# Kernel tuning notes

Hardware: AMD Instinct MI355X
Metric: run time of the kernel (lower is better)

Reference implementation:

```python
import jax, jax.numpy as jnp
import numpy as np

B, LQ, LK, DQ, DK, DV = 8, 2048, 2048, 1024, 1024, 1024
TOP_K = 64
NEG_INF = float('-inf')


def setup_inputs() -> dict:
    key = jax.random.key(0)
    kq, kk, kv, km, kw = jax.random.split(key, 5)
    queries = jax.random.normal(kq, (B, LQ, DQ), dtype=jnp.float32)
    keys = jax.random.normal(kk, (B, LK, DK), dtype=jnp.float32)
    values = jax.random.normal(kv, (B, LK, DV), dtype=jnp.float32)
    mask = jax.random.randint(km, (B, LQ, LK), 0, 2, dtype=jnp.int32)
    # nn.Linear(query_dim, key_dim, bias=False) weight: [key_dim, query_dim]
    W = jax.random.normal(kw, (DK, DQ), dtype=jnp.float32) / np.sqrt(DQ)
    return {"queries": queries, "keys": keys, "values": values,
            "mask": mask, "W": W, "top_k": TOP_K}


def reference(queries, keys, values, mask, W, top_k):
    # scores = (queries @ W.T) @ keys^T  -> [B, LQ, LK]  (method='general')
    q_proj = jnp.einsum('bqd,kd->bqk', queries, W)  # [B, LQ, DK]
    scores = jnp.einsum('bqd,btd->bqt', q_proj, keys)  # [B, LQ, LK]
    scores = jnp.where(mask == 0, NEG_INF, scores)
    alphas = jax.nn.softmax(scores, axis=-1)
    alphas = jnp.where(jnp.isnan(alphas), 0.0, alphas)  # fully-masked rows -> 0
    # top-k: zero out non-top-k probabilities, then re-softmax over the
    # resulting tensor (zeros contribute exp(0)=1, matching torch semantics)
    _, idx = jax.lax.top_k(alphas, top_k)  # [B, LQ, top_k]
    b_idx = jnp.arange(alphas.shape[0])[:, None, None]
    q_idx = jnp.arange(alphas.shape[1])[None, :, None]
    topk_mask = jnp.zeros(alphas.shape, alphas.dtype).at[b_idx, q_idx, idx].set(1.0)
    alphas = jnp.where(topk_mask == 0, 0.0, alphas)
    alphas = jax.nn.softmax(alphas, axis=-1)
    alphas = jnp.where(jnp.isnan(alphas), 0.0, alphas)
    # dropout_rate = 0.0 -> identity
    return jnp.einsum('bqt,btd->bqd', alphas, values)  # [B, LQ, DV]
```

## Files before the change

### kernel.cpp

```cpp
#include <hip/hip_runtime.h>
#include <math.h>

#define BATCH 8
#define SEQ   2048
#define DIM   1024
#define TOPK  64
#define NEGMASK -1e30f
#define CAND_THRESH 16.0f
#define CAP 28

typedef _Float16 f16;
typedef _Float16 f16x8 __attribute__((ext_vector_type(8)));
typedef float f32x4 __attribute__((ext_vector_type(4)));

__device__ __forceinline__ void async_load16(const void* g, void* l) {
  __builtin_amdgcn_global_load_lds(
      (const __attribute__((address_space(1))) void*)g,
      (__attribute__((address_space(3))) void*)l, 16, 0, 0);
}

__global__ __launch_bounds__(256) void pack_mask_kernel(
    const int4* __restrict__ mask4, unsigned long long* __restrict__ mb) {
  const int wave = threadIdx.x >> 6, lane = threadIdx.x & 63;
  const size_t nGrp = (size_t)16384 * 8;
  for (size_t g = (size_t)blockIdx.x * 8 + wave * 2; g < nGrp; g += 2048 * 8) {
    int4 v0 = mask4[g * 64 + lane];
    int4 v1 = mask4[(g + 1) * 64 + lane];
    unsigned long long a0 = __ballot(v0.x != 0);
    unsigned long long a1 = __ballot(v0.y != 0);
    unsigned long long a2 = __ballot(v0.z != 0);
    unsigned long long a3 = __ballot(v0.w != 0);
    unsigned long long b0 = __ballot(v1.x != 0);
    unsigned long long b1 = __ballot(v1.y != 0);
    unsigned long long b2 = __ballot(v1.z != 0);
    unsigned long long b3 = __ballot(v1.w != 0);
    if (lane == 0) {
      mb[g * 4 + 0] = a0; mb[g * 4 + 1] = a1;
      mb[g * 4 + 2] = a2; mb[g * 4 + 3] = a3;
      mb[g * 4 + 4] = b0; mb[g * 4 + 5] = b1;
      mb[g * 4 + 6] = b2; mb[g * 4 + 7] = b3;
    }
  }
}

__global__ __launch_bounds__(256) void colsum_partial_kernel(
    const float* __restrict__ values, float* __restrict__ partial) {
  int bid = blockIdx.x;
  int tc = bid >> 5;
  int b  = (bid >> 2) & 7;
  int dg = bid & 3;
  int d  = dg * 256 + threadIdx.x;
  const float* vp = values + ((size_t)b * SEQ + (size_t)tc * 256) * DIM + d;
  float s = 0.f;
  #pragma unroll 8
  for (int t = 0; t < 256; ++t) s += vp[(size_t)t * DIM];
  partial[((size_t)tc * BATCH + b) * DIM + d] = s;
}

__global__ __launch_bounds__(256) void colsum_reduce_kernel(
    const float* __restrict__ partial, float* __restrict__ colsum) {
  int idx = blockIdx.x * 256 + threadIdx.x;
  float s = 0.f;
  #pragma unroll
  for (int tc = 0; tc < 8; ++tc) s += partial[(size_t)tc * 8192 + idx];
  colsum[idx] = s;
}

__global__ __launch_bounds__(256) void cvt_f32_to_f16(
    const float* __restrict__ in, f16* __restrict__ out, int n) {
  int i = (blockIdx.x * 256 + threadIdx.x) * 4;
  if (i >= n) return;
  float4 v = *(const float4*)(in + i);
  union { f16 h[4]; uint2 u; } pk;
  pk.h[0] = (f16)v.x; pk.h[1] = (f16)v.y; pk.h[2] = (f16)v.z; pk.h[3] = (f16)v.w;
  *(uint2*)(out + i) = pk.u;
}


#define GEMM_PROLOGUE(APTR, BPTR)                                           \
  const int tid = threadIdx.x;                                              \
  const int wave = tid >> 6, lane = tid & 63;                               \
  const int wm = (wave >> 1) * 64, wn = (wave & 1) * 64;                    \
  const int r0 = wave * 32 + (lane >> 2);                                   \
  const int c16 = (lane & 3) ^ ((r0 >> 1) & 3);                            \
  const f16* srcA0 = (APTR) + (size_t)(m0 + r0) * DIM + c16 * 8;           \
  const f16* srcA1 = (APTR) + (size_t)(m0 + r0 + 16) * DIM + c16 * 8;      \
  const f16* srcB0 = (BPTR) + (size_t)(n0 + r0) * DIM + c16 * 8;           \
  const f16* srcB1 = (BPTR) + (size_t)(n0 + r0 + 16) * DIM + c16 * 8;      \
  int offA[4], offB[4];                                                     \
  _Pragma("unroll")                                                         \
  for (int i = 0; i < 4; ++i) {                                             \
    int r = wm + i * 16 + (lane & 15);                                      \
    offA[i] = r * 64 + ((lane >> 4) ^ ((r >> 1) & 3)) * 16;                 \
    int rn = wn + i * 16 + (lane & 15);                                     \
    offB[i] = rn * 64 + ((lane >> 4) ^ ((rn >> 1) & 3)) * 16;               \
  }                                                                         \
  f32x4 acc[4][4];                                                          \
  _Pragma("unroll")                                                         \
  for (int i = 0; i < 4; ++i)                                               \
    _Pragma("unroll")                                                       \
    for (int j = 0; j < 4; ++j)                                             \
      acc[i][j] = (f32x4){0.f, 0.f, 0.f, 0.f};                              \
                                    \
  async_load16(srcA0, smA + wave * 2048);                                   \
  async_load16(srcA1, smA + wave * 2048 + 1024);                            \
  async_load16(srcB0, smB + wave * 2048);                                   \
  async_load16(srcB1, smB + wave * 2048 + 1024);                            \
  __syncthreads();                                                          \
  int cur = 0;                                                              \
  for (int k0 = 0; k0 < DIM; k0 += 32) {                                    \
    const int nxt = cur ^ 1;                                                \
    if (k0 + 32 < DIM) {                                                    \
      async_load16(srcA0 + k0 + 32, smA + nxt * 8192 + wave * 2048);        \
      async_load16(srcA1 + k0 + 32, smA + nxt * 8192 + wave * 2048 + 1024); \
      async_load16(srcB0 + k0 + 32, smB + nxt * 8192 + wave * 2048);        \
      async_load16(srcB1 + k0 + 32, smB + nxt * 8192 + wave * 2048 + 1024); \
    }                                                                       \
    f16x8 af[4], bf[4];                                                     \
    _Pragma("unroll")                                                       \
    for (int i = 0; i < 4; ++i) {                                           \
      af[i] = *(const f16x8*)(smA + cur * 8192 + offA[i]);                  \
      bf[i] = *(const f16x8*)(smB + cur * 8192 + offB[i]);                  \
    }                                                                       \
    _Pragma("unroll")                                                       \
    for (int i = 0; i < 4; ++i)                                             \
      _Pragma("unroll")                                                     \
      for (int j = 0; j < 4; ++j)                                           \
        acc[i][j] = __builtin_amdgcn_mfma_f32_16x16x32_f16(                 \
            af[i], bf[j], acc[i][j], 0, 0, 0);                              \
    __syncthreads();   \
    cur = nxt;                                                              \
  }

__global__ __launch_bounds__(256, 3) void gemm_qproj(
    const f16* __restrict__ A, const f16* __restrict__ Bw,
    f16* __restrict__ C) {
  __shared__ __align__(128) char smA[16384];
  __shared__ __align__(128) char smB[16384];
  const int swz = (blockIdx.x & 7) * 128 + (blockIdx.x >> 3);
  const int m0 = (swz >> 3) * 128;
  const int n0 = (swz & 7) * 128;
  GEMM_PROLOGUE(A, Bw)
  const int cr = m0 + wm + (lane >> 4) * 4;
  const int cc = n0 + wn + (lane & 15);
  #pragma unroll
  for (int i = 0; i < 4; ++i)
    #pragma unroll
    for (int j = 0; j < 4; ++j)
      #pragma unroll
      for (int reg = 0; reg < 4; ++reg)
        C[(size_t)(cr + i * 16 + reg) * DIM + cc + j * 16] = (f16)acc[i][j][reg];
}

__global__ __launch_bounds__(256, 3) void gemm_scores(
    const f16* __restrict__ QP, const f16* __restrict__ K16,
    const unsigned long long* __restrict__ maskbits,
    float2* __restrict__ cand,
    int* __restrict__ counts) {
  __shared__ __align__(128) char smA[16384];
  __shared__ __align__(128) char smB[16384];
  const int swz = (blockIdx.x & 7) * 256 + (blockIdx.x >> 3);
  const int m0 = (swz >> 4) * 128;
  const int n0 = (swz & 15) * 128;
  const int b  = m0 >> 11;
  const f16* Bk = K16 + (size_t)b * SEQ * DIM;
  GEMM_PROLOGUE(QP, Bk)

  const int g  = lane >> 4;
  const int lc = lane & 15;

  const int grp = (n0 + wn) >> 8;
  const int basebit = ((n0 + wn) & 255) >> 2;
  #pragma unroll
  for (int i = 0; i < 4; ++i)
    #pragma unroll
    for (int reg = 0; reg < 4; ++reg) {
      const int r = wm + i * 16 + g * 4 + reg;
      const unsigned long long mw =
          maskbits[(size_t)(m0 + r) * 32 + grp * 4 + (lc & 3)];
      #pragma unroll
      for (int j = 0; j < 4; ++j)
        if (!((mw >> (basebit + j * 4 + (lc >> 2))) & 1ull))
          acc[i][j][reg] = NEGMASK;
    }

  float* hm = (float*)smA;
  #pragma unroll
  for (int i = 0; i < 4; ++i)
    #pragma unroll
    for (int reg = 0; reg < 4; ++reg) {
      const int r = wm + i * 16 + g * 4 + reg;
      float m4 = fmaxf(fmaxf(acc[i][0][reg], acc[i][1][reg]),
                       fmaxf(acc[i][2][reg], acc[i][3][reg]));
      #pragma unroll
      for (int off = 8; off >= 1; off >>= 1) m4 = fmaxf(m4, __shfl_xor(m4, off));
      if (lc == 0) hm[r * 2 + (wn >> 6)] = m4;
    }
  __syncthreads();

  const int pairbase = (n0 >> 7) * 2 + (wn >> 6);
  #pragma unroll
  for (int i = 0; i < 4; ++i)
    #pragma unroll
    for (int reg = 0; reg < 4; ++reg) {
      const int r = wm + i * 16 + g * 4 + reg;
      const float tm = fmaxf(hm[r * 2], hm[r * 2 + 1]);
      const float thresh = fmaxf(tm - CAND_THRESH, -1e29f);
      float2* slot = cand + ((size_t)(m0 + r) * 32 + pairbase) * CAP;
      int cnt = 0;
      #pragma unroll
      for (int j = 0; j < 4; ++j) {
        const float s = acc[i][j][reg];
        const bool c = s > thresh;
        const unsigned long long bal = __ballot(c);
        const int seg = (int)((bal >> (g * 16)) & 0xFFFFull);
        const int pos = cnt + __popc(seg & ((1 << lc) - 1));
        if (c && pos < CAP) {
          float2 e; e.x = s; e.y = __int_as_float(n0 + wn + j * 16 + lc);
          slot[pos] = e;
        }
        cnt += __popc(seg);
      }
      if (lc == 0) counts[(size_t)(m0 + r) * 32 + pairbase] = cnt < CAP ? cnt : CAP;
    }
}

__global__ __launch_bounds__(512) void topk_kernel(
    const float2* __restrict__ cand,
    const int*    __restrict__ counts,
    const float*  __restrict__ values,
    const float*  __restrict__ colsum,
    float* __restrict__ out)
{
  __shared__ float ssc[8][128];
  __shared__ int   sidx[8][128];
  const int wave = threadIdx.x >> 6;
  const int lane = threadIdx.x & 63;
  const int grow = blockIdx.x * 8 + wave;
  const int b    = grow >> 11;
  float* msc = ssc[wave];
  int*   mix = sidx[wave];

  int cnt_p = 0;
  if (lane < 32) cnt_p = counts[(size_t)grow * 32 + lane];
  const float2* myslots = cand + ((size_t)grow * 32 + lane) * CAP;

  float mv = -3e38f;
  for (int k = 0; k < cnt_p; ++k) mv = fmaxf(mv, myslots[k].x);
  #pragma unroll
  for (int off = 32; off > 0; off >>= 1) mv = fmaxf(mv, __shfl_xor(mv, off));
  const bool dead = (mv <= -1e29f);

  float total_g = 0.f;
  f32x4 oacc[4];
  #pragma unroll
  for (int j = 0; j < 4; ++j) oacc[j] = (f32x4){0.f, 0.f, 0.f, 0.f};
  const float* vbase = values + (size_t)b * SEQ * DIM;

  if (!dead) {
    const float thresh = mv - CAND_THRESH;
    int f = 0; float zp = 0.f;
    for (int k = 0; k < cnt_p; ++k) {
      float s = myslots[k].x;
      if (s > thresh) { ++f; zp += __expf(s - mv); }
    }
    int incl = f;
    #pragma unroll
    for (int off = 1; off < 64; off <<= 1) {
      int t = __shfl_up(incl, off);
      if (lane >= off) incl += t;
    }
    const int base = incl - f;
    const int F = __shfl(incl, 63);
    #pragma unroll
    for (int off = 32; off > 0; off >>= 1) zp += __shfl_xor(zp, off);
    const float Z = zp;
    int w = 0;
    for (int k = 0; k < cnt_p; ++k) {
      float2 cv = myslots[k];
      if (cv.x > thresh) {
        int p = base + w;
        if (p < 128) { msc[p] = cv.x; mix[p] = __float_as_int(cv.y); }
        ++w;
      }
    }
    asm volatile("s_waitcnt lgkmcnt(0)" ::: "memory");

    if (F <= TOPK) {
      for (int c = 0; c < F; ++c) {
        float g = expm1f(__expf(msc[c] - mv) / Z);
        total_g += g;
        const float* vrow = vbase + (size_t)mix[c] * DIM;
        #pragma unroll
        for (int j = 0; j < 4; ++j) {
          f32x4 v = *(const f32x4*)(vrow + j * 256 + lane * 4);
          #pragma unroll
          for (int e = 0; e < 4; ++e) oacc[j][e] = fmaf(g, v[e], oacc[j][e]);
        }
      }
    } else {
      const int nlist = F < 128 ? F : 128;
      for (int itk = 0; itk < TOPK; ++itk) {
        float bv = -3e38f; int bi = 1 << 30; int bsl = -1;
        #pragma unroll
        for (int h = 0; h < 2; ++h) {
          int sl = lane + h * 64;
          if (sl < nlist) {
            float v = msc[sl]; int id = mix[sl];
            if (v > bv || (v == bv && id < bi)) { bv = v; bi = id; bsl = sl; }
          }
        }
        #pragma unroll
        for (int off = 32; off > 0; off >>= 1) {
          float ov = __shfl_xor(bv, off);
          int   oi = __shfl_xor(bi, off);
          int   os = __shfl_xor(bsl, off);
          if (ov > bv || (ov == bv && oi < bi)) { bv = ov; bi = oi; bsl = os; }
        }
        if (bv <= -1e29f) break;
        float g = expm1f(__expf(bv - mv) / Z);
        total_g += g;
        const float* vrow = vbase + (size_t)bi * DIM;
        #pragma unroll
        for (int j = 0; j < 4; ++j) {
          f32x4 v = *(const f32x4*)(vrow + j * 256 + lane * 4);
          #pragma unroll
          for (int e = 0; e < 4; ++e) oacc[j][e] = fmaf(g, v[e], oacc[j][e]);
        }
        if (lane == 0) msc[bsl] = -3e38f;
        asm volatile("s_waitcnt lgkmcnt(0)" ::: "memory");
      }
    }
  }

  const float inv = 1.0f / (2048.0f + total_g);
  const float* cs = colsum + (size_t)b * DIM;
  float* orow = out + (size_t)grow * DIM;
  #pragma unroll
  for (int j = 0; j < 4; ++j) {
    f32x4 c = *(const f32x4*)(cs + j * 256 + lane * 4);
    f32x4 o;
    #pragma unroll
    for (int e = 0; e < 4; ++e) o[e] = (c[e] + oacc[j][e]) * inv;
    *(f32x4*)(orow + j * 256 + lane * 4) = o;
  }
}

extern "C" void kernel_launch(void* const* d_in, const int* in_sizes, int n_in,
                              void* d_out, int out_size, void* d_ws, size_t ws_size,
                              hipStream_t stream) {
  const float* queries = (const float*)d_in[0];
  const float* keys    = (const float*)d_in[1];
  const float* values  = (const float*)d_in[2];
  const int*   mask    = (const int*)d_in[3];
  const float* W       = (const float*)d_in[4];
  float* out = (float*)d_out;

  char* base = (char*)d_ws;
  float2* cand   = (float2*)base;
  f16*   q16     = (f16*)base;
  f16*   w16     = (f16*)(base + (size_t)32 * 1024 * 1024);
  int*   counts  = (int*)(base + (size_t)112 * 1024 * 1024);
  unsigned long long* maskbits =
      (unsigned long long*)(base + (size_t)114 * 1024 * 1024);
  f16*   qp16    = (f16*)(base + (size_t)128 * 1024 * 1024);
  f16*   k16     = (f16*)(base + (size_t)160 * 1024 * 1024);
  float* colsum  = (float*)(base + (size_t)192 * 1024 * 1024);
  float* partial = colsum + 8192;

  pack_mask_kernel<<<2048, 256, 0, stream>>>((const int4*)mask, maskbits);
  colsum_partial_kernel<<<256, 256, 0, stream>>>(values, partial);
  colsum_reduce_kernel<<<32, 256, 0, stream>>>(partial, colsum);
  cvt_f32_to_f16<<<16384, 256, 0, stream>>>(queries, q16, 16384 * 1024);
  cvt_f32_to_f16<<<1024, 256, 0, stream>>>(W, w16, 1024 * 1024);
  gemm_qproj<<<1024, 256, 0, stream>>>(q16, w16, qp16);
  cvt_f32_to_f16<<<16384, 256, 0, stream>>>(keys, k16, 16384 * 1024);
  gemm_scores<<<2048, 256, 0, stream>>>(qp16, k16, maskbits, cand, counts);
  topk_kernel<<<2048, 512, 0, stream>>>(cand, counts, values, colsum, out);
}
```

Before: 317.8 us.

## Shrink GEMM tiles to 128x64 and merge prep kernels into two launches

Both GEMMs now use 128x64 output tiles with 24 KB of shared memory and a launch bound of 4 blocks. Each wave owns a 32x64 strip, so the cross-wave max exchange and extra barrier in the scores epilogue go away, and the candidate threshold becomes the max of each 64-column chunk. The mask packing, column sums and f32-to-f16 conversions are folded into two multi-role kernels to cut launch count and let independent prep work overlap. In exchange each A tile is reloaded from global memory twice as often, and the per-chunk threshold may admit more candidates before the CAP limit.

```diff
diff --git a/kernel.cpp b/kernel.cpp
--- a/kernel.cpp
+++ b/kernel.cpp
@@ -19,209 +19,203 @@
       (__attribute__((address_space(3))) void*)l, 16, 0, 0);
 }
 
-__global__ __launch_bounds__(256) void pack_mask_kernel(
-    const int4* __restrict__ mask4, unsigned long long* __restrict__ mb) {
-  const int wave = threadIdx.x >> 6, lane = threadIdx.x & 63;
-  const size_t nGrp = (size_t)16384 * 8;
-  for (size_t g = (size_t)blockIdx.x * 8 + wave * 2; g < nGrp; g += 2048 * 8) {
-    int4 v0 = mask4[g * 64 + lane];
-    int4 v1 = mask4[(g + 1) * 64 + lane];
-    unsigned long long a0 = __ballot(v0.x != 0);
-    unsigned long long a1 = __ballot(v0.y != 0);
-    unsigned long long a2 = __ballot(v0.z != 0);
-    unsigned long long a3 = __ballot(v0.w != 0);
-    unsigned long long b0 = __ballot(v1.x != 0);
-    unsigned long long b1 = __ballot(v1.y != 0);
-    unsigned long long b2 = __ballot(v1.z != 0);
-    unsigned long long b3 = __ballot(v1.w != 0);
-    if (lane == 0) {
-      mb[g * 4 + 0] = a0; mb[g * 4 + 1] = a1;
-      mb[g * 4 + 2] = a2; mb[g * 4 + 3] = a3;
-      mb[g * 4 + 4] = b0; mb[g * 4 + 5] = b1;
-      mb[g * 4 + 6] = b2; mb[g * 4 + 7] = b3;
-    }
-  }
-}
-
-__global__ __launch_bounds__(256) void colsum_partial_kernel(
-    const float* __restrict__ values, float* __restrict__ partial) {
-  int bid = blockIdx.x;
-  int tc = bid >> 5;
-  int b  = (bid >> 2) & 7;
-  int dg = bid & 3;
-  int d  = dg * 256 + threadIdx.x;
-  const float* vp = values + ((size_t)b * SEQ + (size_t)tc * 256) * DIM + d;
-  float s = 0.f;
-  #pragma unroll 8
-  for (int t = 0; t < 256; ++t) s += vp[(size_t)t * DIM];
-  partial[((size_t)tc * BATCH + b) * DIM + d] = s;
-}
-
-__global__ __launch_bounds__(256) void colsum_reduce_kernel(
-    const float* __restrict__ partial, float* __restrict__ colsum) {
-  int idx = blockIdx.x * 256 + threadIdx.x;
-  float s = 0.f;
-  #pragma unroll
-  for (int tc = 0; tc < 8; ++tc) s += partial[(size_t)tc * 8192 + idx];
-  colsum[idx] = s;
-}
-
-__global__ __launch_bounds__(256) void cvt_f32_to_f16(
-    const float* __restrict__ in, f16* __restrict__ out, int n) {
-  int i = (blockIdx.x * 256 + threadIdx.x) * 4;
-  if (i >= n) return;
-  float4 v = *(const float4*)(in + i);
-  union { f16 h[4]; uint2 u; } pk;
-  pk.h[0] = (f16)v.x; pk.h[1] = (f16)v.y; pk.h[2] = (f16)v.z; pk.h[3] = (f16)v.w;
-  *(uint2*)(out + i) = pk.u;
-}
-
+__global__ __launch_bounds__(256) void prep1_kernel(
+    const float* __restrict__ queries, const float* __restrict__ W,
+    const int4* __restrict__ mask4, const float* __restrict__ values,
+    f16* __restrict__ q16, f16* __restrict__ w16,
+    unsigned long long* __restrict__ mb, float* __restrict__ partial) {
+  const int blk = blockIdx.x;
+  if (blk < 16384) {
+    int i = (blk * 256 + threadIdx.x) * 4;
+    float4 v = *(const float4*)(queries + i);
+    union { f16 h[4]; uint2 u; } pk;
+    pk.h[0] = (f16)v.x; pk.h[1] = (f16)v.y; pk.h[2] = (f16)v.z; pk.h[3] = (f16)v.w;
+    *(uint2*)(q16 + i) = pk.u;
+  } else if (blk < 17408) {
+    int i = ((blk - 16384) * 256 + threadIdx.x) * 4;
+    float4 v = *(const float4*)(W + i);
+    union { f16 h[4]; uint2 u; } pk;
+    pk.h[0] = (f16)v.x; pk.h[1] = (f16)v.y; pk.h[2] = (f16)v.z; pk.h[3] = (f16)v.w;
+    *(uint2*)(w16 + i) = pk.u;
+  } else if (blk < 19456) {
+    const int bid = blk - 17408;
+    const int wave = threadIdx.x >> 6, lane = threadIdx.x & 63;
+    const size_t nGrp = (size_t)16384 * 8;
+    for (size_t g = (size_t)bid * 8 + wave * 2; g < nGrp; g += 2048 * 8) {
+      int4 v0 = mask4[g * 64 + lane];
+      int4 v1 = mask4[(g + 1) * 64 + lane];
+      unsigned long long a0 = __ballot(v0.x != 0);
+      unsigned long long a1 = __ballot(v0.y != 0);
+      unsigned long long a2 = __ballot(v0.z != 0);
+      unsigned long long a3 = __ballot(v0.w != 0);
+      unsigned long long b0 = __ballot(v1.x != 0);
+      unsigned long long b1 = __ballot(v1.y != 0);
+      unsigned long long b2 = __ballot(v1.z != 0);
+      unsigned long long b3 = __ballot(v1.w != 0);
+      if (lane == 0) {
+        mb[g * 4 + 0] = a0; mb[g * 4 + 1] = a1;
+        mb[g * 4 + 2] = a2; mb[g * 4 + 3] = a3;
+        mb[g * 4 + 4] = b0; mb[g * 4 + 5] = b1;
+        mb[g * 4 + 6] = b2; mb[g * 4 + 7] = b3;
+      }
+    }
+  } else {
+    const int bid = blk - 19456;
+    int tc = bid >> 5;
+    int b  = (bid >> 2) & 7;
+    int dg = bid & 3;
+    int d  = dg * 256 + threadIdx.x;
+    const float* vp = values + ((size_t)b * SEQ + (size_t)tc * 256) * DIM + d;
+    float s = 0.f;
+    #pragma unroll 8
+    for (int t = 0; t < 256; ++t) s += vp[(size_t)t * DIM];
+    partial[((size_t)tc * BATCH + b) * DIM + d] = s;
+  }
+}
+
+__global__ __launch_bounds__(256) void prep2_kernel(
+    const float* __restrict__ keys, const float* __restrict__ partial,
+    f16* __restrict__ k16, float* __restrict__ colsum) {
+  const int blk = blockIdx.x;
+  if (blk < 16384) {
+    int i = (blk * 256 + threadIdx.x) * 4;
+    float4 v = *(const float4*)(keys + i);
+    union { f16 h[4]; uint2 u; } pk;
+    pk.h[0] = (f16)v.x; pk.h[1] = (f16)v.y; pk.h[2] = (f16)v.z; pk.h[3] = (f16)v.w;
+    *(uint2*)(k16 + i) = pk.u;
+  } else {
+    int idx = (blk - 16384) * 256 + threadIdx.x;
+    float s = 0.f;
+    #pragma unroll
+    for (int tc = 0; tc < 8; ++tc) s += partial[(size_t)tc * 8192 + idx];
+    colsum[idx] = s;
+  }
+}
+
+
+#define STAGEK(KOFF, BUF)                                                   \
+  async_load16(srcA0 + (KOFF), sm + (BUF) * 12288 + wave * 2048);           \
+  async_load16(srcA1 + (KOFF), sm + (BUF) * 12288 + wave * 2048 + 1024);    \
+  async_load16(srcB0 + (KOFF), sm + (BUF) * 12288 + 8192 + wave * 1024);
 
 #define GEMM_PROLOGUE(APTR, BPTR)                                           \
   const int tid = threadIdx.x;                                              \
   const int wave = tid >> 6, lane = tid & 63;                               \
-  const int wm = (wave >> 1) * 64, wn = (wave & 1) * 64;                    \
+  const int lcq = lane >> 4, l15 = lane & 15;                               \
   const int r0 = wave * 32 + (lane >> 2);                                   \
   const int c16 = (lane & 3) ^ ((r0 >> 1) & 3);                            \
+  const int r0b = wave * 16 + (lane >> 2);                                  \
+  const int c16b = (lane & 3) ^ ((r0b >> 1) & 3);                          \
   const f16* srcA0 = (APTR) + (size_t)(m0 + r0) * DIM + c16 * 8;           \
   const f16* srcA1 = (APTR) + (size_t)(m0 + r0 + 16) * DIM + c16 * 8;      \
-  const f16* srcB0 = (BPTR) + (size_t)(n0 + r0) * DIM + c16 * 8;           \
-  const f16* srcB1 = (BPTR) + (size_t)(n0 + r0 + 16) * DIM + c16 * 8;      \
-  int offA[4], offB[4];                                                     \
+  const f16* srcB0 = (BPTR) + (size_t)(n0 + r0b) * DIM + c16b * 8;         \
+  int offA[2], offB[4];                                                     \
   _Pragma("unroll")                                                         \
-  for (int i = 0; i < 4; ++i) {                                             \
-    int r = wm + i * 16 + (lane & 15);                                      \
-    offA[i] = r * 64 + ((lane >> 4) ^ ((r >> 1) & 3)) * 16;                 \
-    int rn = wn + i * 16 + (lane & 15);                                     \
-    offB[i] = rn * 64 + ((lane >> 4) ^ ((rn >> 1) & 3)) * 16;               \
+  for (int fm = 0; fm < 2; ++fm) {                                          \
+    int r = wave * 32 + fm * 16 + l15;                                      \
+    offA[fm] = r * 64 + (lcq ^ ((r >> 1) & 3)) * 16;                        \
   }                                                                         \
-  f32x4 acc[4][4];                                                          \
   _Pragma("unroll")                                                         \
-  for (int i = 0; i < 4; ++i)                                               \
+  for (int fn = 0; fn < 4; ++fn) {                                          \
+    int rn = fn * 16 + l15;                                                 \
+    offB[fn] = 8192 + rn * 64 + (lcq ^ ((rn >> 1) & 3)) * 16;               \
+  }                                                                         \
+  f32x4 acc[2][4];                                                          \
+  _Pragma("unroll")                                                         \
+  for (int i = 0; i < 2; ++i)                                               \
     _Pragma("unroll")                                                       \
     for (int j = 0; j < 4; ++j)                                             \
       acc[i][j] = (f32x4){0.f, 0.f, 0.f, 0.f};                              \
-                                    \
-  async_load16(srcA0, smA + wave * 2048);                                   \
-  async_load16(srcA1, smA + wave * 2048 + 1024);                            \
-  async_load16(srcB0, smB + wave * 2048);                                   \
-  async_load16(srcB1, smB + wave * 2048 + 1024);                            \
+  STAGEK(0, 0)                                                              \
   __syncthreads();                                                          \
   int cur = 0;                                                              \
   for (int k0 = 0; k0 < DIM; k0 += 32) {                                    \
     const int nxt = cur ^ 1;                                                \
-    if (k0 + 32 < DIM) {                                                    \
-      async_load16(srcA0 + k0 + 32, smA + nxt * 8192 + wave * 2048);        \
-      async_load16(srcA1 + k0 + 32, smA + nxt * 8192 + wave * 2048 + 1024); \
-      async_load16(srcB0 + k0 + 32, smB + nxt * 8192 + wave * 2048);        \
-      async_load16(srcB1 + k0 + 32, smB + nxt * 8192 + wave * 2048 + 1024); \
-    }                                                                       \
-    f16x8 af[4], bf[4];                                                     \
+    if (k0 + 32 < DIM) { STAGEK(k0 + 32, nxt) }                             \
+    f16x8 af[2], bf[4];                                                     \
     _Pragma("unroll")                                                       \
-    for (int i = 0; i < 4; ++i) {                                           \
-      af[i] = *(const f16x8*)(smA + cur * 8192 + offA[i]);                  \
-      bf[i] = *(const f16x8*)(smB + cur * 8192 + offB[i]);                  \
-    }                                                                       \
+    for (int fm = 0; fm < 2; ++fm)                                          \
+      af[fm] = *(const f16x8*)(sm + cur * 12288 + offA[fm]);                \
     _Pragma("unroll")                                                       \
-    for (int i = 0; i < 4; ++i)                                             \
+    for (int fn = 0; fn < 4; ++fn)                                          \
+      bf[fn] = *(const f16x8*)(sm + cur * 12288 + offB[fn]);                \
+    _Pragma("unroll")                                                       \
+    for (int fm = 0; fm < 2; ++fm)                                          \
       _Pragma("unroll")                                                     \
-      for (int j = 0; j < 4; ++j)                                           \
-        acc[i][j] = __builtin_amdgcn_mfma_f32_16x16x32_f16(                 \
-            af[i], bf[j], acc[i][j], 0, 0, 0);                              \
-    __syncthreads();   \
+      for (int fn = 0; fn < 4; ++fn)                                        \
+        acc[fm][fn] = __builtin_amdgcn_mfma_f32_16x16x32_f16(               \
+            af[fm], bf[fn], acc[fm][fn], 0, 0, 0);                          \
+    __syncthreads();                                                        \
     cur = nxt;                                                              \
   }
 
-__global__ __launch_bounds__(256, 3) void gemm_qproj(
+__global__ __launch_bounds__(256, 4) void gemm_qproj(
     const f16* __restrict__ A, const f16* __restrict__ Bw,
     f16* __restrict__ C) {
-  __shared__ __align__(128) char smA[16384];
-  __shared__ __align__(128) char smB[16384];
-  const int swz = (blockIdx.x & 7) * 128 + (blockIdx.x >> 3);
-  const int m0 = (swz >> 3) * 128;
-  const int n0 = (swz & 7) * 128;
+  __shared__ __align__(128) char sm[24576];
+  const int swz = (blockIdx.x & 7) * 256 + (blockIdx.x >> 3);
+  const int m0 = (swz >> 4) * 128;
+  const int n0 = (swz & 15) * 64;
   GEMM_PROLOGUE(A, Bw)
-  const int cr = m0 + wm + (lane >> 4) * 4;
-  const int cc = n0 + wn + (lane & 15);
-  #pragma unroll
-  for (int i = 0; i < 4; ++i)
-    #pragma unroll
-    for (int j = 0; j < 4; ++j)
+  #pragma unroll
+  for (int fm = 0; fm < 2; ++fm)
+    #pragma unroll
+    for (int reg = 0; reg < 4; ++reg) {
+      const int cr = m0 + wave * 32 + fm * 16 + lcq * 4 + reg;
       #pragma unroll
-      for (int reg = 0; reg < 4; ++reg)
-        C[(size_t)(cr + i * 16 + reg) * DIM + cc + j * 16] = (f16)acc[i][j][reg];
-}
-
-__global__ __launch_bounds__(256, 3) void gemm_scores(
+      for (int fn = 0; fn < 4; ++fn)
+        C[(size_t)cr * DIM + n0 + fn * 16 + l15] = (f16)acc[fm][fn][reg];
+    }
+}
+
+__global__ __launch_bounds__(256, 4) void gemm_scores(
     const f16* __restrict__ QP, const f16* __restrict__ K16,
     const unsigned long long* __restrict__ maskbits,
     float2* __restrict__ cand,
     int* __restrict__ counts) {
-  __shared__ __align__(128) char smA[16384];
-  __shared__ __align__(128) char smB[16384];
-  const int swz = (blockIdx.x & 7) * 256 + (blockIdx.x >> 3);
-  const int m0 = (swz >> 4) * 128;
-  const int n0 = (swz & 15) * 128;
+  __shared__ __align__(128) char sm[24576];
+  const int swz = (blockIdx.x & 7) * 512 + (blockIdx.x >> 3);
+  const int m0 = (swz >> 5) * 128;
+  const int n0 = (swz & 31) * 64;
   const int b  = m0 >> 11;
   const f16* Bk = K16 + (size_t)b * SEQ * DIM;
   GEMM_PROLOGUE(QP, Bk)
 
-  const int g  = lane >> 4;
-  const int lc = lane & 15;
-
-  const int grp = (n0 + wn) >> 8;
-  const int basebit = ((n0 + wn) & 255) >> 2;
-  #pragma unroll
-  for (int i = 0; i < 4; ++i)
+  const int grp = n0 >> 8;
+  const int basebit = (n0 & 255) >> 2;
+  const int pairb = n0 >> 6;
+  #pragma unroll
+  for (int fm = 0; fm < 2; ++fm)
     #pragma unroll
     for (int reg = 0; reg < 4; ++reg) {
-      const int r = wm + i * 16 + g * 4 + reg;
-      const unsigned long long mw =
-          maskbits[(size_t)(m0 + r) * 32 + grp * 4 + (lc & 3)];
+      const int rloc = wave * 32 + fm * 16 + lcq * 4 + reg;
+      const size_t grow = (size_t)m0 + rloc;
+      const unsigned long long mw = maskbits[grow * 32 + grp * 4 + (l15 & 3)];
       #pragma unroll
-      for (int j = 0; j < 4; ++j)
-        if (!((mw >> (basebit + j * 4 + (lc >> 2))) & 1ull))
-          acc[i][j][reg] = NEGMASK;
-    }
-
-  float* hm = (float*)smA;
-  #pragma unroll
-  for (int i = 0; i < 4; ++i)
-    #pragma unroll
-    for (int reg = 0; reg < 4; ++reg) {
-      const int r = wm + i * 16 + g * 4 + reg;
-      float m4 = fmaxf(fmaxf(acc[i][0][reg], acc[i][1][reg]),
-                       fmaxf(acc[i][2][reg], acc[i][3][reg]));
+      for (int fn = 0; fn < 4; ++fn)
+        if (!((mw >> (basebit + fn * 4 + (l15 >> 2))) & 1ull))
+          acc[fm][fn][reg] = NEGMASK;
+      float m4 = fmaxf(fmaxf(acc[fm][0][reg], acc[fm][1][reg]),
+                       fmaxf(acc[fm][2][reg], acc[fm][3][reg]));
       #pragma unroll
       for (int off = 8; off >= 1; off >>= 1) m4 = fmaxf(m4, __shfl_xor(m4, off));
-      if (lc == 0) hm[r * 2 + (wn >> 6)] = m4;
-    }
-  __syncthreads();
-
-  const int pairbase = (n0 >> 7) * 2 + (wn >> 6);
-  #pragma unroll
-  for (int i = 0; i < 4; ++i)
-    #pragma unroll
-    for (int reg = 0; reg < 4; ++reg) {
-      const int r = wm + i * 16 + g * 4 + reg;
-      const float tm = fmaxf(hm[r * 2], hm[r * 2 + 1]);
-      const float thresh = fmaxf(tm - CAND_THRESH, -1e29f);
-      float2* slot = cand + ((size_t)(m0 + r) * 32 + pairbase) * CAP;
+      const float thresh = fmaxf(m4 - CAND_THRESH, -1e29f);
+      float2* slot = cand + (grow * 32 + pairb) * CAP;
       int cnt = 0;
       #pragma unroll
-      for (int j = 0; j < 4; ++j) {
-        const float s = acc[i][j][reg];
+      for (int fn = 0; fn < 4; ++fn) {
+        const float s = acc[fm][fn][reg];
         const bool c = s > thresh;
         const unsigned long long bal = __ballot(c);
-        const int seg = (int)((bal >> (g * 16)) & 0xFFFFull);
-        const int pos = cnt + __popc(seg & ((1 << lc) - 1));
+        const int seg = (int)((bal >> (lcq * 16)) & 0xFFFFull);
+        const int pos = cnt + __popc(seg & ((1 << l15) - 1));
         if (c && pos < CAP) {
-          float2 e; e.x = s; e.y = __int_as_float(n0 + wn + j * 16 + lc);
+          float2 e; e.x = s; e.y = __int_as_float(n0 + fn * 16 + l15);
           slot[pos] = e;
         }
         cnt += __popc(seg);
       }
-      if (lc == 0) counts[(size_t)(m0 + r) * 32 + pairbase] = cnt < CAP ? cnt : CAP;
+      if (l15 == 0) counts[grow * 32 + pairb] = cnt < CAP ? cnt : CAP;
     }
 }
 
@@ -368,13 +362,10 @@
   float* colsum  = (float*)(base + (size_t)192 * 1024 * 1024);
   float* partial = colsum + 8192;
 
-  pack_mask_kernel<<<2048, 256, 0, stream>>>((const int4*)mask, maskbits);
-  colsum_partial_kernel<<<256, 256, 0, stream>>>(values, partial);
-  colsum_reduce_kernel<<<32, 256, 0, stream>>>(partial, colsum);
-  cvt_f32_to_f16<<<16384, 256, 0, stream>>>(queries, q16, 16384 * 1024);
-  cvt_f32_to_f16<<<1024, 256, 0, stream>>>(W, w16, 1024 * 1024);
-  gemm_qproj<<<1024, 256, 0, stream>>>(q16, w16, qp16);
-  cvt_f32_to_f16<<<16384, 256, 0, stream>>>(keys, k16, 16384 * 1024);
-  gemm_scores<<<2048, 256, 0, stream>>>(qp16, k16, maskbits, cand, counts);
+  prep1_kernel<<<19712, 256, 0, stream>>>(queries, W, (const int4*)mask, values,
+                                          q16, w16, maskbits, partial);
+  prep2_kernel<<<16416, 256, 0, stream>>>(keys, partial, k16, colsum);
+  gemm_qproj<<<2048, 256, 0, stream>>>(q16, w16, qp16);
+  gemm_scores<<<4096, 256, 0, stream>>>(qp16, k16, maskbits, cand, counts);
   topk_kernel<<<2048, 512, 0, stream>>>(cand, counts, values, colsum, out);
 }
```

New measurement: 350.0 us. 10.1% more time.

## Merge preprocessing kernels and relax GEMM barrier waits for deeper prefetch overlap

Applied to the files above, without the earlier changes.

Combines the mask packing, column-sum partials, and query/W conversions into one launch, and the key conversion plus column-sum reduce into a second. This cuts the number of small kernel launches and lets independent memory-bound work run concurrently. The column-sum partial pass is also split finer (64 rows per block). The GEMM main loop replaces __syncthreads with explicit vmcnt waits and raw barriers, so the next tile's async loads can stay in flight while the current tile is consumed. This relies on hand-managed waitcnt correctness for the LDS async loads.

```diff
diff --git a/kernel.cpp b/kernel.cpp
--- a/kernel.cpp
+++ b/kernel.cpp
@@ -19,63 +19,85 @@
       (__attribute__((address_space(3))) void*)l, 16, 0, 0);
 }
 
-__global__ __launch_bounds__(256) void pack_mask_kernel(
-    const int4* __restrict__ mask4, unsigned long long* __restrict__ mb) {
-  const int wave = threadIdx.x >> 6, lane = threadIdx.x & 63;
-  const size_t nGrp = (size_t)16384 * 8;
-  for (size_t g = (size_t)blockIdx.x * 8 + wave * 2; g < nGrp; g += 2048 * 8) {
-    int4 v0 = mask4[g * 64 + lane];
-    int4 v1 = mask4[(g + 1) * 64 + lane];
-    unsigned long long a0 = __ballot(v0.x != 0);
-    unsigned long long a1 = __ballot(v0.y != 0);
-    unsigned long long a2 = __ballot(v0.z != 0);
-    unsigned long long a3 = __ballot(v0.w != 0);
-    unsigned long long b0 = __ballot(v1.x != 0);
-    unsigned long long b1 = __ballot(v1.y != 0);
-    unsigned long long b2 = __ballot(v1.z != 0);
-    unsigned long long b3 = __ballot(v1.w != 0);
-    if (lane == 0) {
-      mb[g * 4 + 0] = a0; mb[g * 4 + 1] = a1;
-      mb[g * 4 + 2] = a2; mb[g * 4 + 3] = a3;
-      mb[g * 4 + 4] = b0; mb[g * 4 + 5] = b1;
-      mb[g * 4 + 6] = b2; mb[g * 4 + 7] = b3;
-    }
-  }
-}
-
-__global__ __launch_bounds__(256) void colsum_partial_kernel(
-    const float* __restrict__ values, float* __restrict__ partial) {
-  int bid = blockIdx.x;
-  int tc = bid >> 5;
-  int b  = (bid >> 2) & 7;
-  int dg = bid & 3;
-  int d  = dg * 256 + threadIdx.x;
-  const float* vp = values + ((size_t)b * SEQ + (size_t)tc * 256) * DIM + d;
-  float s = 0.f;
-  #pragma unroll 8
-  for (int t = 0; t < 256; ++t) s += vp[(size_t)t * DIM];
-  partial[((size_t)tc * BATCH + b) * DIM + d] = s;
-}
-
-__global__ __launch_bounds__(256) void colsum_reduce_kernel(
-    const float* __restrict__ partial, float* __restrict__ colsum) {
-  int idx = blockIdx.x * 256 + threadIdx.x;
-  float s = 0.f;
-  #pragma unroll
-  for (int tc = 0; tc < 8; ++tc) s += partial[(size_t)tc * 8192 + idx];
-  colsum[idx] = s;
-}
-
-__global__ __launch_bounds__(256) void cvt_f32_to_f16(
-    const float* __restrict__ in, f16* __restrict__ out, int n) {
-  int i = (blockIdx.x * 256 + threadIdx.x) * 4;
-  if (i >= n) return;
-  float4 v = *(const float4*)(in + i);
-  union { f16 h[4]; uint2 u; } pk;
-  pk.h[0] = (f16)v.x; pk.h[1] = (f16)v.y; pk.h[2] = (f16)v.z; pk.h[3] = (f16)v.w;
-  *(uint2*)(out + i) = pk.u;
-}
-
+__global__ __launch_bounds__(256) void prep1_kernel(
+    const float* __restrict__ queries, const float* __restrict__ W,
+    const int4* __restrict__ mask4, const float* __restrict__ values,
+    f16* __restrict__ q16, f16* __restrict__ w16,
+    unsigned long long* __restrict__ mb, float* __restrict__ partial) {
+  const int blk = blockIdx.x;
+  if (blk < 16384) {
+    int i = (blk * 256 + threadIdx.x) * 4;
+    float4 v = *(const float4*)(queries + i);
+    union { f16 h[4]; uint2 u; } pk;
+    pk.h[0] = (f16)v.x; pk.h[1] = (f16)v.y; pk.h[2] = (f16)v.z; pk.h[3] = (f16)v.w;
+    *(uint2*)(q16 + i) = pk.u;
+  } else if (blk < 17408) {
+    int i = ((blk - 16384) * 256 + threadIdx.x) * 4;
+    float4 v = *(const float4*)(W + i);
+    union { f16 h[4]; uint2 u; } pk;
+    pk.h[0] = (f16)v.x; pk.h[1] = (f16)v.y; pk.h[2] = (f16)v.z; pk.h[3] = (f16)v.w;
+    *(uint2*)(w16 + i) = pk.u;
+  } else if (blk < 19456) {
+    const int bid = blk - 17408;
+    const int wave = threadIdx.x >> 6, lane = threadIdx.x & 63;
+    const size_t nGrp = (size_t)16384 * 8;
+    for (size_t g = (size_t)bid * 8 + wave * 2; g < nGrp; g += 2048 * 8) {
+      int4 v0 = mask4[g * 64 + lane];
+      int4 v1 = mask4[(g + 1) * 64 + lane];
+      unsigned long long a0 = __ballot(v0.x != 0);
+      unsigned long long a1 = __ballot(v0.y != 0);
+      unsigned long long a2 = __ballot(v0.z != 0);
+      unsigned long long a3 = __ballot(v0.w != 0);
+      unsigned long long b0 = __ballot(v1.x != 0);
+      unsigned long long b1 = __ballot(v1.y != 0);
+      unsigned long long b2 = __ballot(v1.z != 0);
+      unsigned long long b3 = __ballot(v1.w != 0);
+      if (lane == 0) {
+        mb[g * 4 + 0] = a0; mb[g * 4 + 1] = a1;
+        mb[g * 4 + 2] = a2; mb[g * 4 + 3] = a3;
+        mb[g * 4 + 4] = b0; mb[g * 4 + 5] = b1;
+        mb[g * 4 + 6] = b2; mb[g * 4 + 7] = b3;
+      }
+    }
+  } else {
+    const int bid = blk - 19456;
+    int tc = bid >> 5;
+    int b  = (bid >> 2) & 7;
+    int dg = bid & 3;
+    int d  = dg * 256 + threadIdx.x;
+    const float* vp = values + ((size_t)b * SEQ + (size_t)tc * 64) * DIM + d;
+    float s = 0.f;
+    #pragma unroll 8
+    for (int t = 0; t < 64; ++t) s += vp[(size_t)t * DIM];
+    partial[((size_t)tc * BATCH + b) * DIM + d] = s;
+  }
+}
+
+__global__ __launch_bounds__(256) void prep2_kernel(
+    const float* __restrict__ keys, const float* __restrict__ partial,
+    f16* __restrict__ k16, float* __restrict__ colsum) {
+  const int blk = blockIdx.x;
+  if (blk < 16384) {
+    int i = (blk * 256 + threadIdx.x) * 4;
+    float4 v = *(const float4*)(keys + i);
+    union { f16 h[4]; uint2 u; } pk;
+    pk.h[0] = (f16)v.x; pk.h[1] = (f16)v.y; pk.h[2] = (f16)v.z; pk.h[3] = (f16)v.w;
+    *(uint2*)(k16 + i) = pk.u;
+  } else {
+    int idx = (blk - 16384) * 256 + threadIdx.x;
+    float s = 0.f;
+    #pragma unroll
+    for (int tc = 0; tc < 32; ++tc) s += partial[(size_t)tc * 8192 + idx];
+    colsum[idx] = s;
+  }
+}
+
+
+#define STAGEK(KOFF, BUF)                                                   \
+  async_load16(srcA0 + (KOFF), smA + (BUF) * 8192 + wave * 2048);           \
+  async_load16(srcA1 + (KOFF), smA + (BUF) * 8192 + wave * 2048 + 1024);    \
+  async_load16(srcB0 + (KOFF), smB + (BUF) * 8192 + wave * 2048);           \
+  async_load16(srcB1 + (KOFF), smB + (BUF) * 8192 + wave * 2048 + 1024);
 
 #define GEMM_PROLOGUE(APTR, BPTR)                                           \
   const int tid = threadIdx.x;                                              \
@@ -101,21 +123,18 @@
     _Pragma("unroll")                                                       \
     for (int j = 0; j < 4; ++j)                                             \
       acc[i][j] = (f32x4){0.f, 0.f, 0.f, 0.f};                              \
-                                    \
-  async_load16(srcA0, smA + wave * 2048);                                   \
-  async_load16(srcA1, smA + wave * 2048 + 1024);                            \
-  async_load16(srcB0, smB + wave * 2048);                                   \
-  async_load16(srcB1, smB + wave * 2048 + 1024);                            \
-  __syncthreads();                                                          \
+  STAGEK(0, 0)                                                              \
   int cur = 0;                                                              \
   for (int k0 = 0; k0 < DIM; k0 += 32) {                                    \
     const int nxt = cur ^ 1;                                                \
     if (k0 + 32 < DIM) {                                                    \
-      async_load16(srcA0 + k0 + 32, smA + nxt * 8192 + wave * 2048);        \
-      async_load16(srcA1 + k0 + 32, smA + nxt * 8192 + wave * 2048 + 1024); \
-      async_load16(srcB0 + k0 + 32, smB + nxt * 8192 + wave * 2048);        \
-      async_load16(srcB1 + k0 + 32, smB + nxt * 8192 + wave * 2048 + 1024); \
+      STAGEK(k0 + 32, nxt)                                                  \
+      asm volatile("s_waitcnt vmcnt(4)" ::: "memory");                      \
+    } else {                                                                \
+      asm volatile("s_waitcnt vmcnt(0)" ::: "memory");                      \
     }                                                                       \
+    __builtin_amdgcn_s_barrier();                                           \
+    asm volatile("" ::: "memory");                                          \
     f16x8 af[4], bf[4];                                                     \
     _Pragma("unroll")                                                       \
     for (int i = 0; i < 4; ++i) {                                           \
@@ -128,7 +147,8 @@
       for (int j = 0; j < 4; ++j)                                           \
         acc[i][j] = __builtin_amdgcn_mfma_f32_16x16x32_f16(                 \
             af[i], bf[j], acc[i][j], 0, 0, 0);                              \
-    __syncthreads();   \
+    asm volatile("" ::: "memory");                                          \
+    __builtin_amdgcn_s_barrier();                                           \
     cur = nxt;                                                              \
   }
 
@@ -363,18 +383,15 @@
   int*   counts  = (int*)(base + (size_t)112 * 1024 * 1024);
   unsigned long long* maskbits =
       (unsigned long long*)(base + (size_t)114 * 1024 * 1024);
+  float* colsum  = (float*)(base + (size_t)118 * 1024 * 1024);
+  float* partial = (float*)(base + (size_t)119 * 1024 * 1024);
   f16*   qp16    = (f16*)(base + (size_t)128 * 1024 * 1024);
   f16*   k16     = (f16*)(base + (size_t)160 * 1024 * 1024);
-  float* colsum  = (float*)(base + (size_t)192 * 1024 * 1024);
-  float* partial = colsum + 8192;
-
-  pack_mask_kernel<<<2048, 256, 0, stream>>>((const int4*)mask, maskbits);
-  colsum_partial_kernel<<<256, 256, 0, stream>>>(values, partial);
-  colsum_reduce_kernel<<<32, 256, 0, stream>>>(partial, colsum);
-  cvt_f32_to_f16<<<16384, 256, 0, stream>>>(queries, q16, 16384 * 1024);
-  cvt_f32_to_f16<<<1024, 256, 0, stream>>>(W, w16, 1024 * 1024);
+
+  prep1_kernel<<<20480, 256, 0, stream>>>(queries, W, (const int4*)mask, values,
+                                          q16, w16, maskbits, partial);
+  prep2_kernel<<<16416, 256, 0, stream>>>(keys, partial, k16, colsum);
   gemm_qproj<<<1024, 256, 0, stream>>>(q16, w16, qp16);
-  cvt_f32_to_f16<<<16384, 256, 0, stream>>>(keys, k16, 16384 * 1024);
   gemm_scores<<<2048, 256, 0, stream>>>(qp16, k16, maskbits, cand, counts);
   topk_kernel<<<2048, 512, 0, stream>>>(cand, counts, values, colsum, out);
 }
```

New measurement: 301.1 us. 1.06x faster.
